# Performance work log

Measured on AMD Instinct MI355X. Metric: run time of the kernel, lower is better.

Reference implementation:

```python
import jax, jax.numpy as jnp
import numpy as np

N = 16000   # query points
M = 16000   # support points
NB = 32     # neighbors per query
A = 4       # kanchor (SO(2)/z-axis discrete anchors, kanchor<10 branch)
K = 15      # kernel points
CIN = 32
COUT = 32
RADIUS = 1.0
KP_EXTENT = 0.6


def _make_kernel_points(key):
    # KPConv-style kernel points inside a sphere of radius 0.66*RADIUS, first point at center
    kp = jax.random.normal(key, (K, 3), dtype=jnp.float32)
    kp = kp / (jnp.linalg.norm(kp, axis=-1, keepdims=True) + 1e-8)
    r = jax.random.uniform(jax.random.fold_in(key, 1), (K, 1), dtype=jnp.float32) ** (1.0 / 3.0)
    kp = kp * r * (0.66 * RADIUS)
    return kp.at[0].set(0.0)


def _make_anchors():
    # kanchor=4 -> rotations about z by 2*pi*a/A (E2PN get_anchors for kanchor<10)
    ang = 2.0 * jnp.pi * jnp.arange(A, dtype=jnp.float32) / A
    c, s = jnp.cos(ang), jnp.sin(ang)
    z = jnp.zeros_like(c)
    o = jnp.ones_like(c)
    return jnp.stack([c, -s, z, s, c, z, z, z, o], axis=-1).reshape(A, 3, 3)


def setup_inputs() -> dict:
    key = jax.random.key(0)
    k1, k2, k3, k4, k5, k6 = jax.random.split(key, 6)
    q_pts = jax.random.uniform(k1, (N, 3), dtype=jnp.float32) * 0.5
    s_pts = jax.random.uniform(k2, (M, 3), dtype=jnp.float32) * 0.5
    neighb_inds = jax.random.randint(k3, (N, NB), 0, M, dtype=jnp.int32)
    x = jax.random.normal(k4, (M, A, CIN), dtype=jnp.float32)
    kernel_points = _make_kernel_points(k5)
    anchors = _make_anchors()
    # kaiming-uniform-ish init of the (K, C_in, C_out) separable conv weights
    bound = float(np.sqrt(6.0 / ((1 + 5) * CIN)))
    weights = jax.random.uniform(k6, (K, CIN, COUT), dtype=jnp.float32,
                                 minval=-bound, maxval=bound)
    return {"q_pts": q_pts, "s_pts": s_pts, "neighb_inds": neighb_inds, "x": x,
            "kernel_points": kernel_points, "anchors": anchors, "weights": weights}


def reference(q_pts, s_pts, neighb_inds, x, kernel_points, anchors, weights):
    # neighbor gather, centered on query points: [N, NB, 3]
    neighbors = s_pts[neighb_inds] - q_pts[:, None, :]
    # rotate kernel points by each anchor: [A, K, 3]
    rot_kp = jnp.einsum('aij,kj->aki', anchors, kernel_points)
    # squared distances via |n|^2 + |kp|^2 - 2 n.kp (avoids [A,N,NB,K,3] blowup)
    n2 = jnp.sum(neighbors * neighbors, axis=-1)          # [N, NB]
    k2 = jnp.sum(rot_kp * rot_kp, axis=-1)                # [A, K]
    cross = jnp.einsum('nbj,akj->anbk', neighbors, rot_kp)
    sq_distances = n2[None, :, :, None] + k2[:, None, None, :] - 2.0 * cross  # [A,N,NB,K]
    # linear KP influence, clamped at 0
    all_weights = jnp.clip(1.0 - jnp.sqrt(jnp.maximum(sq_distances, 1e-12)) / KP_EXTENT,
                           0.0, None)                      # [A, N, NB, K]
    # gather neighbor features: [N, NB, A, C_in]
    neighb_x = x[neighb_inds]
    # weight neighbors onto kernel points (sum aggregation): [A, N, K, C_in]
    weighted_feats = jnp.einsum('anbk,nbac->ankc', all_weights, neighb_x)
    # per-kernel-point small GEMMs, summed over K: [N, A, C_out]
    out = jnp.einsum('ankc,kcd->nad', weighted_feats, weights)
    return out
```

## Files before the change

kernel.cpp:

```cpp
#include <hip/hip_runtime.h>


typedef short bf16x8 __attribute__((ext_vector_type(8)));
typedef float f32x4  __attribute__((ext_vector_type(4)));

__device__ __forceinline__ unsigned short f2bf(float f) {
    unsigned u = __builtin_bit_cast(unsigned, f);
    return (unsigned short)((u + 0x8000u) >> 16);
}
__device__ __forceinline__ float bf2f(unsigned short h) {
    return __builtin_bit_cast(float, (unsigned)h << 16);
}
__device__ __forceinline__ unsigned pack2bf(float hi, float lo) {
    unsigned uh = __builtin_bit_cast(unsigned, hi) + 0x8000u;
    unsigned ul = __builtin_bit_cast(unsigned, lo) + 0x8000u;
    return __builtin_amdgcn_perm(uh, ul, 0x07060302u);
}
__device__ __forceinline__ void bfsplit(float v, unsigned short& h, unsigned short& l) {
    h = f2bf(v);
    l = f2bf(v - bf2f(h));
}

__global__ void prep_w(const float* __restrict__ W, unsigned short* __restrict__ Wp) {
    const int idx = blockIdx.x * 256 + threadIdx.x;
    const int kk = idx >> 10, d = (idx >> 5) & 31, e = idx & 31;
    const int kcs = kk * 32 + e;
    const int c = kcs >> 4, k = kcs & 15;
    const float v = (k < 15) ? W[(k * 32 + c) * 32 + d] : 0.0f;
    Wp[idx] = f2bf(v);
}

__global__ void prep_x(const float* __restrict__ x, unsigned short* __restrict__ xb) {
    const int i = (blockIdx.x * 256 + threadIdx.x) * 8;
    const float4 v0 = *(const float4*)&x[i];
    const float4 v1 = *(const float4*)&x[i + 4];
    uint4 u;
    u.x = pack2bf(v0.y, v0.x); u.y = pack2bf(v0.w, v0.z);
    u.z = pack2bf(v1.y, v1.x); u.w = pack2bf(v1.w, v1.z);
    *(uint4*)&xb[i] = u;
}

__global__ __launch_bounds__(256) void kpconv_mfma(
    const float* __restrict__ q_pts,
    const float* __restrict__ s_pts,
    const int*   __restrict__ inds,
    const unsigned short* __restrict__ xb,
    const float* __restrict__ kp,
    const float* __restrict__ anchors,
    const unsigned short* __restrict__ Wp,
    float*       __restrict__ out)
{
    __shared__ __align__(16) unsigned short xa_s[16384];
    __shared__ __align__(16) unsigned short nbr32[3072];
    __shared__ __align__(16) unsigned short zz[128];

    const int t  = threadIdx.x;
    const int n0 = blockIdx.x * 4;
    const int a = t >> 6, lane = t & 63, l15 = lane & 15, quad = lane >> 4;

    bf16x8 rkb;
    {
        float rx = 0.f, ry = 0.f, rz = 0.f, k2 = 1e30f;
        if (l15 < 15) {
            const float kx = kp[l15*3+0], ky = kp[l15*3+1], kz = kp[l15*3+2];
            const float* R = anchors + a * 9;
            rx = R[0]*kx + R[1]*ky + R[2]*kz;
            ry = R[3]*kx + R[4]*ky + R[5]*kz;
            rz = R[6]*kx + R[7]*ky + R[8]*kz;
            k2 = rx*rx + ry*ry + rz*rz;
        }
        unsigned short k2h,k2l, Rxh,Rxl, Ryh,Ryl, Rzh,Rzl;
        bfsplit(k2, k2h, k2l);
        bfsplit(-2.0f*rx, Rxh, Rxl);
        bfsplit(-2.0f*ry, Ryh, Ryl);
        bfsplit(-2.0f*rz, Rzh, Rzl);
        const unsigned ONE = 0x3F80u;
        uint4 u;
        if (quad == 0) {
            u.x = (unsigned)k2h | ((unsigned)k2l << 16);
            u.y = (unsigned)Rxh | ((unsigned)Rxl << 16);
            u.z = (unsigned)Rxh | ((unsigned)Ryh << 16);
            u.w = (unsigned)Ryl | ((unsigned)Ryh << 16);
        } else if (quad == 1) {
            u.x = (unsigned)Rzh | ((unsigned)Rzl << 16);
            u.y = (unsigned)Rzh | (ONE << 16);
            u.z = ONE;
            u.w = 0u;
        } else {
            u.x = u.y = u.z = u.w = 0u;
        }
        rkb = __builtin_bit_cast(bf16x8, u);
    }

    if (t < 128) {
        const int q = t >> 5, b = t & 31;
        const int idx = inds[(n0 + q) * 32 + b];
        const float nx = s_pts[idx*3+0] - q_pts[(n0+q)*3+0];
        const float ny = s_pts[idx*3+1] - q_pts[(n0+q)*3+1];
        const float nz = s_pts[idx*3+2] - q_pts[(n0+q)*3+2];
        const float n2 = nx*nx + ny*ny + nz*nz;
        unsigned short nxh,nxl, nyh,nyl, nzh,nzl, n2h,n2l;
        bfsplit(nx, nxh, nxl); bfsplit(ny, nyh, nyl);
        bfsplit(nz, nzh, nzl); bfsplit(n2, n2h, n2l);
        const unsigned ONE = 0x3F80u;
        uint4 lo, hi;
        lo.x = ONE | (ONE << 16);
        lo.y = (unsigned)nxh | ((unsigned)nxh << 16);
        lo.z = (unsigned)nxl | ((unsigned)nyh << 16);
        lo.w = (unsigned)nyh | ((unsigned)nyl << 16);
        hi.x = (unsigned)nzh | ((unsigned)nzh << 16);
        hi.y = (unsigned)nzl | ((unsigned)n2h << 16);
        hi.z = (unsigned)n2l;
        hi.w = 0u;
        unsigned short* p = &nbr32[(q * 32 + b) * 24];
        *(uint4*)(p)     = lo;
        *(uint4*)(p + 8) = hi;
    } else if (t < 144) {
        *(uint4*)&zz[(t - 128) * 8] = make_uint4(0,0,0,0);
    }

    {
        const int c4 = t & 7, bg = (t >> 3) & 7, q = t >> 6;
        const int4 rows = *(const int4*)&inds[(n0 + q) * 32 + 4 * bg];
        const int fcs   = c4 & 3;
        const int slotb = ((bg & 3) ^ fcs) * 8 + (bg >> 2) * 4;
        unsigned short* base = &xa_s[(q * 32) * 32 + slotb];
        #pragma unroll
        for (int aa = 0; aa < 4; ++aa) {
            const uint2 r0 = *(const uint2*)&xb[rows.x * 128 + aa * 32 + c4 * 4];
            const uint2 r1 = *(const uint2*)&xb[rows.y * 128 + aa * 32 + c4 * 4];
            const uint2 r2 = *(const uint2*)&xb[rows.z * 128 + aa * 32 + c4 * 4];
            const uint2 r3 = *(const uint2*)&xb[rows.w * 128 + aa * 32 + c4 * 4];
            unsigned short* pa = base + aa * 4096;
            uint2 w;
            w.x = __builtin_amdgcn_perm(r1.x, r0.x, 0x05040100u);
            w.y = __builtin_amdgcn_perm(r3.x, r2.x, 0x05040100u);
            *(uint2*)&pa[(4 * c4 + 0) * 32] = w;
            w.x = __builtin_amdgcn_perm(r1.x, r0.x, 0x07060302u);
            w.y = __builtin_amdgcn_perm(r3.x, r2.x, 0x07060302u);
            *(uint2*)&pa[(4 * c4 + 1) * 32] = w;
            w.x = __builtin_amdgcn_perm(r1.y, r0.y, 0x05040100u);
            w.y = __builtin_amdgcn_perm(r3.y, r2.y, 0x05040100u);
            *(uint2*)&pa[(4 * c4 + 2) * 32] = w;
            w.x = __builtin_amdgcn_perm(r1.y, r0.y, 0x07060302u);
            w.y = __builtin_amdgcn_perm(r3.y, r2.y, 0x07060302u);
            *(uint2*)&pa[(4 * c4 + 3) * 32] = w;
        }
    }
    __syncthreads();

    const int fc = (l15 >> 2) & 3;
    unsigned short* wfb = &xa_s[a * 4096];
    const f32x4 zacc = {0.f, 0.f, 0.f, 0.f};

    #pragma unroll
    for (int q = 0; q < 4; ++q) {
        const unsigned short* aX = (quad < 2)
            ? &nbr32[(q * 32 + l15) * 24 + (quad & 1) * 8]       : &zz[l15 * 8];
        const unsigned short* aY = (quad < 2)
            ? &nbr32[(q * 32 + 16 + l15) * 24 + (quad & 1) * 8]  : &zz[l15 * 8];
        const f32x4 s0 = __builtin_amdgcn_mfma_f32_16x16x32_bf16(*(const bf16x8*)aX, rkb, zacc, 0, 0, 0);
        const f32x4 s1 = __builtin_amdgcn_mfma_f32_16x16x32_bf16(*(const bf16x8*)aY, rkb, zacc, 0, 0, 0);
        float w8[8];
        #pragma unroll
        for (int j = 0; j < 4; ++j) {
            w8[j]     = fmaxf(fmaf(sqrtf(fmaxf(s0[j], 1e-12f)), -1.6666667f, 1.0f), 0.0f);
            w8[4 + j] = fmaxf(fmaf(sqrtf(fmaxf(s1[j], 1e-12f)), -1.6666667f, 1.0f), 0.0f);
        }
        uint4 uu;
        uu.x = pack2bf(w8[1], w8[0]); uu.y = pack2bf(w8[3], w8[2]);
        uu.z = pack2bf(w8[5], w8[4]); uu.w = pack2bf(w8[7], w8[6]);
        const bf16x8 afr = __builtin_bit_cast(bf16x8, uu);

        const bf16x8 b0 = *(const bf16x8*)&xa_s[((a*4 + q)*32 + l15)      * 32 + 8 * (quad ^ fc)];
        const bf16x8 b1 = *(const bf16x8*)&xa_s[((a*4 + q)*32 + l15 + 16) * 32 + 8 * (quad ^ fc)];
        f32x4 d0 = zacc, d1 = zacc;
        d0 = __builtin_amdgcn_mfma_f32_16x16x32_bf16(afr, b0, d0, 0, 0, 0);
        d1 = __builtin_amdgcn_mfma_f32_16x16x32_bf16(afr, b1, d1, 0, 0, 0);
        uint2 s0p, s1p;
        s0p.x = pack2bf(d0[1], d0[0]); s0p.y = pack2bf(d0[3], d0[2]);
        s1p.x = pack2bf(d1[1], d1[0]); s1p.y = pack2bf(d1[3], d1[2]);
        *(uint2*)&wfb[q*512 + (( l15       * 16 + quad * 4) ^ (q * 16))] = s0p;
        *(uint2*)&wfb[q*512 + (((l15 + 16) * 16 + quad * 4) ^ (q * 16))] = s1p;
    }

    const int qq = l15 & 3;
    f32x4 o0 = zacc, o1 = zacc;
    #pragma unroll
    for (int kk = 0; kk < 16; ++kk) {
        const bf16x8 a2 = *(const bf16x8*)&wfb[qq*512 + ((kk*32 + quad*8) ^ (qq*16))];
        const bf16x8 w0 = *(const bf16x8*)&Wp[kk*1024 + l15*32 + quad*8];
        const bf16x8 w1 = *(const bf16x8*)&Wp[kk*1024 + (l15+16)*32 + quad*8];
        o0 = __builtin_amdgcn_mfma_f32_16x16x32_bf16(a2, w0, o0, 0, 0, 0);
        o1 = __builtin_amdgcn_mfma_f32_16x16x32_bf16(a2, w1, o1, 0, 0, 0);
    }
    if (quad == 0) {
        #pragma unroll
        for (int r = 0; r < 4; ++r) {
            out[((n0 + r) * 4 + a) * 32 + l15]      = o0[r];
            out[((n0 + r) * 4 + a) * 32 + 16 + l15] = o1[r];
        }
    }
}

extern "C" void kernel_launch(void* const* d_in, const int* in_sizes, int n_in,
                              void* d_out, int out_size, void* d_ws, size_t ws_size,
                              hipStream_t stream) {
    const float* q_pts   = (const float*)d_in[0];
    const float* s_pts   = (const float*)d_in[1];
    const int*   inds    = (const int*)d_in[2];
    const float* x       = (const float*)d_in[3];
    const float* kp      = (const float*)d_in[4];
    const float* anchors = (const float*)d_in[5];
    const float* weights = (const float*)d_in[6];
    float*       out     = (float*)d_out;

    unsigned short* Wp = (unsigned short*)d_ws;
    unsigned short* xb = (unsigned short*)((char*)d_ws + (1 << 16));

    prep_w<<<dim3(64),   dim3(256), 0, stream>>>(weights, Wp);
    prep_x<<<dim3(1000), dim3(256), 0, stream>>>(x, xb);
    kpconv_mfma<<<dim3(4000), dim3(256), 0, stream>>>(
        q_pts, s_pts, inds, xb, kp, anchors, Wp, out);
}
```

Measured before the change: 123.6 us.

## Split final weight GEMM across waves with K-split and LDS reduction

Stage three previously had each wave compute a 4x32 output with only 4 useful rows of 16 in each MFMA. Now each wave computes a full 16-row tile that spans all anchors and queries, over half the kernel-point range, and two waves' partials are summed through LDS. This cuts the MFMA count per wave in the final GEMM at the cost of two extra block barriers and an LDS reduction. The zero-padding LDS buffer is removed by reading real neighbor data rows instead, and a rotation-based swizzle replaces the XOR one.

```diff
diff --git a/kernel.cpp b/kernel.cpp
--- a/kernel.cpp
+++ b/kernel.cpp
@@ -52,7 +52,6 @@
 {
     __shared__ __align__(16) unsigned short xa_s[16384];
     __shared__ __align__(16) unsigned short nbr32[3072];
-    __shared__ __align__(16) unsigned short zz[128];
 
     const int t  = threadIdx.x;
     const int n0 = blockIdx.x * 4;
@@ -103,20 +102,14 @@
         bfsplit(nx, nxh, nxl); bfsplit(ny, nyh, nyl);
         bfsplit(nz, nzh, nzl); bfsplit(n2, n2h, n2l);
         const unsigned ONE = 0x3F80u;
-        uint4 lo, hi;
-        lo.x = ONE | (ONE << 16);
-        lo.y = (unsigned)nxh | ((unsigned)nxh << 16);
-        lo.z = (unsigned)nxl | ((unsigned)nyh << 16);
-        lo.w = (unsigned)nyh | ((unsigned)nyl << 16);
-        hi.x = (unsigned)nzh | ((unsigned)nzh << 16);
-        hi.y = (unsigned)nzl | ((unsigned)n2h << 16);
-        hi.z = (unsigned)n2l;
-        hi.w = 0u;
         unsigned short* p = &nbr32[(q * 32 + b) * 24];
-        *(uint4*)(p)     = lo;
-        *(uint4*)(p + 8) = hi;
-    } else if (t < 144) {
-        *(uint4*)&zz[(t - 128) * 8] = make_uint4(0,0,0,0);
+        *(uint2*)(p)      = make_uint2(ONE | (ONE << 16),
+                                       (unsigned)nxh | ((unsigned)nxh << 16));
+        *(uint2*)(p + 4)  = make_uint2((unsigned)nxl | ((unsigned)nyh << 16),
+                                       (unsigned)nyh | ((unsigned)nyl << 16));
+        *(uint2*)(p + 8)  = make_uint2((unsigned)nzh | ((unsigned)nzh << 16),
+                                       (unsigned)nzl | ((unsigned)n2h << 16));
+        *(uint2*)(p + 12) = make_uint2((unsigned)n2l, 0u);
     }
 
     {
@@ -152,13 +145,12 @@
     const int fc = (l15 >> 2) & 3;
     unsigned short* wfb = &xa_s[a * 4096];
     const f32x4 zacc = {0.f, 0.f, 0.f, 0.f};
+    const int S = a * 8;
 
     #pragma unroll
     for (int q = 0; q < 4; ++q) {
-        const unsigned short* aX = (quad < 2)
-            ? &nbr32[(q * 32 + l15) * 24 + (quad & 1) * 8]       : &zz[l15 * 8];
-        const unsigned short* aY = (quad < 2)
-            ? &nbr32[(q * 32 + 16 + l15) * 24 + (quad & 1) * 8]  : &zz[l15 * 8];
+        const unsigned short* aX = &nbr32[(q * 32 + l15) * 24 + (quad & 1) * 8];
+        const unsigned short* aY = &nbr32[(q * 32 + 16 + l15) * 24 + (quad & 1) * 8];
         const f32x4 s0 = __builtin_amdgcn_mfma_f32_16x16x32_bf16(*(const bf16x8*)aX, rkb, zacc, 0, 0, 0);
         const f32x4 s1 = __builtin_amdgcn_mfma_f32_16x16x32_bf16(*(const bf16x8*)aY, rkb, zacc, 0, 0, 0);
         float w8[8];
@@ -180,25 +172,37 @@
         uint2 s0p, s1p;
         s0p.x = pack2bf(d0[1], d0[0]); s0p.y = pack2bf(d0[3], d0[2]);
         s1p.x = pack2bf(d1[1], d1[0]); s1p.y = pack2bf(d1[3], d1[2]);
-        *(uint2*)&wfb[q*512 + (( l15       * 16 + quad * 4) ^ (q * 16))] = s0p;
-        *(uint2*)&wfb[q*512 + (((l15 + 16) * 16 + quad * 4) ^ (q * 16))] = s1p;
-    }
-
-    const int qq = l15 & 3;
-    f32x4 o0 = zacc, o1 = zacc;
+        const int Sq = S + q * 16;
+        *(uint2*)&wfb[q*512 + ((l15*16       + quad*4 + Sq) & 511)] = s0p;
+        *(uint2*)&wfb[q*512 + ((l15*16 + 256 + quad*4 + Sq) & 511)] = s1p;
+    }
+    __syncthreads();
+
+    const int tile = a & 1;
+    const int kkb  = (a >> 1) * 8;
+    const int a_src = l15 >> 2, qv = l15 & 3;
+    const unsigned short* abase = &xa_s[a_src * 4096 + qv * 512];
+    const int shf = qv * 16 + a_src * 8;
+    f32x4 o = zacc;
     #pragma unroll
-    for (int kk = 0; kk < 16; ++kk) {
-        const bf16x8 a2 = *(const bf16x8*)&wfb[qq*512 + ((kk*32 + quad*8) ^ (qq*16))];
-        const bf16x8 w0 = *(const bf16x8*)&Wp[kk*1024 + l15*32 + quad*8];
-        const bf16x8 w1 = *(const bf16x8*)&Wp[kk*1024 + (l15+16)*32 + quad*8];
-        o0 = __builtin_amdgcn_mfma_f32_16x16x32_bf16(a2, w0, o0, 0, 0, 0);
-        o1 = __builtin_amdgcn_mfma_f32_16x16x32_bf16(a2, w1, o1, 0, 0, 0);
-    }
-    if (quad == 0) {
+    for (int kk2 = 0; kk2 < 8; ++kk2) {
+        const int kk = kkb + kk2;
+        const bf16x8 a2 = *(const bf16x8*)&abase[(kk*32 + quad*8 + shf) & 511];
+        const bf16x8 wv = *(const bf16x8*)&Wp[kk*1024 + (tile*16 + l15)*32 + quad*8];
+        o = __builtin_amdgcn_mfma_f32_16x16x32_bf16(a2, wv, o, 0, 0, 0);
+    }
+    __syncthreads();
+    float4* red4 = (float4*)nbr32;
+    if (a >= 2) {
+        red4[(a - 2) * 64 + lane] = make_float4(o[0], o[1], o[2], o[3]);
+    }
+    __syncthreads();
+    if (a < 2) {
+        const float4 p = red4[a * 64 + lane];
+        o[0] += p.x; o[1] += p.y; o[2] += p.z; o[3] += p.w;
         #pragma unroll
         for (int r = 0; r < 4; ++r) {
-            out[((n0 + r) * 4 + a) * 32 + l15]      = o0[r];
-            out[((n0 + r) * 4 + a) * 32 + 16 + l15] = o1[r];
+            out[((n0 + r) * 4 + quad) * 32 + tile * 16 + l15] = o[r];
         }
     }
 }
```

New measurement: 113.5 us. 8.2% less time.
